# Kernel tuning notes

Hardware: AMD Instinct MI355X
Metric: run time of the kernel (lower is better)

Reference implementation:

```python
import jax, jax.numpy as jnp
import numpy as np

MD = 2        # max_displacement
STRIDE2 = 2   # displacement grid stride -> shifts in {-2, 0, 2}


def conv3x3_same(x, w):
    # x: [B,C,H,W], w: [O,I,3,3], stride 1, padding 1, no bias
    return jax.lax.conv_general_dilated(
        x, w, window_strides=(1, 1), padding=((1, 1), (1, 1)),
        dimension_numbers=("NCHW", "OIHW", "NCHW"))


def correlation(f1, f2):
    # FlowNet-style correlation, kernel_size=1: for each displacement (dy,dx)
    # in {-MD..MD step STRIDE2}^2, per-pixel channel dot product of f1 with
    # shifted f2, normalized by C (sumelems = kernel_size^2 * C).
    B, C, H, W = f1.shape
    f2p = jnp.pad(f2, ((0, 0), (0, 0), (MD, MD), (MD, MD)))
    outs = []
    for dy in range(-MD, MD + 1, STRIDE2):
        for dx in range(-MD, MD + 1, STRIDE2):
            f2s = f2p[:, :, MD + dy:MD + dy + H, MD + dx:MD + dx + W]
            outs.append(jnp.mean(f1 * f2s, axis=1))  # [B,H,W]
    return jnp.stack(outs, axis=1)  # [B, 9, H, W]


def setup_inputs() -> dict:
    key = jax.random.key(0)
    k1, k2, k3 = jax.random.split(key, 3)
    B, C, H, W = 16, 3, 512, 512
    x1 = jax.random.normal(k1, (B, C, H, W), dtype=jnp.float32)
    x2 = jax.random.normal(k2, (B, C, H, W), dtype=jnp.float32)
    # conv1: Conv2d(3, 3, kernel_size=3, bias=False); kaiming-ish scale
    fan_in = C * 3 * 3
    conv_w = jax.random.normal(k3, (3, C, 3, 3), dtype=jnp.float32) * np.float32(np.sqrt(2.0 / fan_in))
    return {"x1": x1, "x2": x2, "conv_w": conv_w}


def reference(x1, x2, conv_w):
    f1 = conv3x3_same(x1, conv_w)
    f2 = conv3x3_same(x2, conv_w)
    return correlation(f1, f2)  # [B, 9, H, W]
```

## Files before the change

kernel.cpp:

```cpp
#include <hip/hip_runtime.h>


#define HH 512
#define WW 512
#define TS 32
#define X2R 38
#define X2S 40
#define X1R 34
#define X1S 36
#define F2R 36
#define F2S 40
#define N2 (3*X2R*X2S)
#define N1 (3*X1R*X1S)
#define NC2 (3*X2R*(X2S/4))
#define NC1 (3*X1R*(X1S/4))

typedef const __attribute__((address_space(1))) void* gas_ptr;
typedef __attribute__((address_space(3))) void* las_ptr;
typedef float f32x4 __attribute__((ext_vector_type(4)));

__global__ __launch_bounds__(256)
void flownetc_fused_kernel(const float* __restrict__ x1,
                           const float* __restrict__ x2,
                           const float* __restrict__ cw,
                           float* __restrict__ out) {
  __shared__ __align__(16) float s_x2[N2];
  __shared__ __align__(16) float s_x1[N1];
  __shared__ __align__(16) float s_f2[3*F2R*F2S];

  const int tid = threadIdx.x;
  const int bid = blockIdx.x;
  const int f   = (bid & 7) * 512 + (bid >> 3);
  const int ox0 = (f & 15) * TS;
  const int oy0 = ((f >> 4) & 15) * TS;
  const int bi  = f >> 8;

  const float* x2b = x2 + (size_t)bi * 3 * HH * WW;
  const float* x1b = x1 + (size_t)bi * 3 * HH * WW;

  for (int q = tid; q < NC2; q += 256) {
    const int colq = q % (X2S / 4);
    const int rp   = q / (X2S / 4);
    const int r    = rp % X2R;
    const int c    = rp / X2R;
    const int gy   = oy0 - 3 + r;
    const int gx0  = ox0 - 3 + colq * 4;
    const float* src = x2b + (size_t)(c * HH + gy) * WW + gx0;
    if ((unsigned)gy < HH && (unsigned)gx0 <= (WW - 4)) {
      __builtin_amdgcn_global_load_lds((gas_ptr)src,
          (las_ptr)(s_x2 + ((q & ~63) << 2)), 16, 0, 0);
    } else {
      const bool rowok = (unsigned)gy < HH;
      float4 v;
      v.x = (rowok && (unsigned)(gx0 + 0) < WW) ? src[0] : 0.f;
      v.y = (rowok && (unsigned)(gx0 + 1) < WW) ? src[1] : 0.f;
      v.z = (rowok && (unsigned)(gx0 + 2) < WW) ? src[2] : 0.f;
      v.w = (rowok && (unsigned)(gx0 + 3) < WW) ? src[3] : 0.f;
      *reinterpret_cast<float4*>(&s_x2[q * 4]) = v;
    }
  }
  for (int q = tid; q < NC1; q += 256) {
    const int colq = q % (X1S / 4);
    const int rp   = q / (X1S / 4);
    const int r    = rp % X1R;
    const int c    = rp / X1R;
    const int gy   = oy0 - 1 + r;
    const int gx0  = ox0 - 1 + colq * 4;
    const float* src = x1b + (size_t)(c * HH + gy) * WW + gx0;
    if ((unsigned)gy < HH && (unsigned)gx0 <= (WW - 4)) {
      __builtin_amdgcn_global_load_lds((gas_ptr)src,
          (las_ptr)(s_x1 + ((q & ~63) << 2)), 16, 0, 0);
    } else {
      const bool rowok = (unsigned)gy < HH;
      float4 v;
      v.x = (rowok && (unsigned)(gx0 + 0) < WW) ? src[0] : 0.f;
      v.y = (rowok && (unsigned)(gx0 + 1) < WW) ? src[1] : 0.f;
      v.z = (rowok && (unsigned)(gx0 + 2) < WW) ? src[2] : 0.f;
      v.w = (rowok && (unsigned)(gx0 + 3) < WW) ? src[3] : 0.f;
      *reinterpret_cast<float4*>(&s_x1[q * 4]) = v;
    }
  }
  __syncthreads();

  for (int run = tid; run < 324; run += 256) {
    const int col0 = (run % 9) * 4;
    const int r    = run / 9;
    float acc[3][4] = {};
    #pragma unroll
    for (int ci = 0; ci < 3; ++ci) {
      float win[3][6];
      #pragma unroll
      for (int ky = 0; ky < 3; ++ky) {
        const float* base = &s_x2[(ci * X2R + r + ky) * X2S + col0];
        const float4 a  = *reinterpret_cast<const float4*>(base);
        const float2 b2 = *reinterpret_cast<const float2*>(base + 4);
        win[ky][0] = a.x; win[ky][1] = a.y; win[ky][2] = a.z; win[ky][3] = a.w;
        win[ky][4] = b2.x; win[ky][5] = b2.y;
      }
      #pragma unroll
      for (int co = 0; co < 3; ++co)
        #pragma unroll
        for (int ky = 0; ky < 3; ++ky)
          #pragma unroll
          for (int kx = 0; kx < 3; ++kx) {
            const float w = cw[((co * 3 + ci) * 3 + ky) * 3 + kx];
            #pragma unroll
            for (int j = 0; j < 4; ++j)
              acc[co][j] += w * win[ky][j + kx];
          }
    }
    const int gy = oy0 - 2 + r;
    #pragma unroll
    for (int j = 0; j < 4; ++j) {
      const int gx = ox0 - 2 + col0 + j;
      if (!((unsigned)gy < HH && (unsigned)gx < WW)) {
        acc[0][j] = 0.f; acc[1][j] = 0.f; acc[2][j] = 0.f;
      }
    }
    #pragma unroll
    for (int co = 0; co < 3; ++co)
      *reinterpret_cast<float4*>(&s_f2[(co * F2R + r) * F2S + col0]) =
          make_float4(acc[co][0], acc[co][1], acc[co][2], acc[co][3]);
  }

  const int py  = tid >> 3;
  const int px0 = (tid & 7) << 2;
  float f1r[3][4] = {};
  #pragma unroll
  for (int ci = 0; ci < 3; ++ci) {
    float win[3][6];
    #pragma unroll
    for (int ky = 0; ky < 3; ++ky) {
      const float* base = &s_x1[(ci * X1R + py + ky) * X1S + px0];
      const float4 a  = *reinterpret_cast<const float4*>(base);
      const float2 b2 = *reinterpret_cast<const float2*>(base + 4);
      win[ky][0] = a.x; win[ky][1] = a.y; win[ky][2] = a.z; win[ky][3] = a.w;
      win[ky][4] = b2.x; win[ky][5] = b2.y;
    }
    #pragma unroll
    for (int co = 0; co < 3; ++co)
      #pragma unroll
      for (int ky = 0; ky < 3; ++ky)
        #pragma unroll
        for (int kx = 0; kx < 3; ++kx) {
          const float w = cw[((co * 3 + ci) * 3 + ky) * 3 + kx];
          #pragma unroll
          for (int j = 0; j < 4; ++j)
            f1r[co][j] += w * win[ky][j + kx];
        }
  }
  __syncthreads();

  float* outp = out + ((size_t)bi * 9 * HH + (oy0 + py)) * WW + ox0 + px0;
  #pragma unroll
  for (int dyi = 0; dyi < 3; ++dyi) {
    float rv[3][8];
    #pragma unroll
    for (int c = 0; c < 3; ++c) {
      const float* base = &s_f2[(c * F2R + py + dyi * 2) * F2S + px0];
      const float4 a = *reinterpret_cast<const float4*>(base);
      const float4 b = *reinterpret_cast<const float4*>(base + 4);
      rv[c][0] = a.x; rv[c][1] = a.y; rv[c][2] = a.z; rv[c][3] = a.w;
      rv[c][4] = b.x; rv[c][5] = b.y; rv[c][6] = b.z; rv[c][7] = b.w;
    }
    #pragma unroll
    for (int dxi = 0; dxi < 3; ++dxi) {
      const int s = dxi * 2;
      f32x4 o;
      o.x = (f1r[0][0]*rv[0][s+0] + f1r[1][0]*rv[1][s+0] + f1r[2][0]*rv[2][s+0]) * (1.f/3.f);
      o.y = (f1r[0][1]*rv[0][s+1] + f1r[1][1]*rv[1][s+1] + f1r[2][1]*rv[2][s+1]) * (1.f/3.f);
      o.z = (f1r[0][2]*rv[0][s+2] + f1r[1][2]*rv[1][s+2] + f1r[2][2]*rv[2][s+2]) * (1.f/3.f);
      o.w = (f1r[0][3]*rv[0][s+3] + f1r[1][3]*rv[1][s+3] + f1r[2][3]*rv[2][s+3]) * (1.f/3.f);
      __builtin_nontemporal_store(o,
          reinterpret_cast<f32x4*>(outp + (size_t)(dyi * 3 + dxi) * HH * WW));
    }
  }
}

extern "C" void kernel_launch(void* const* d_in, const int* in_sizes, int n_in,
                              void* d_out, int out_size, void* d_ws, size_t ws_size,
                              hipStream_t stream) {
  const float* x1 = (const float*)d_in[0];
  const float* x2 = (const float*)d_in[1];
  const float* cw = (const float*)d_in[2];
  float* out = (float*)d_out;

  flownetc_fused_kernel<<<dim3(4096), 256, 0, stream>>>(x1, x2, cw, out);
}
```

Before: 62.03 us.

## Widen tiles to 64x32 with 512 threads and alias x1/f2 shared buffers

Doubles the tile width to 64 columns with 512-thread blocks, which cuts the relative halo overhead of loading x2/x1 and recomputing the f2 convolution on the border. The x1 staging buffer and the f2 result buffer now share one LDS array: f1 is computed first, then after a barrier f2 is written over it. This keeps LDS per block small despite the wider tile. It also folds the 1/3 mean scale into f1 once instead of applying it per output. The cost is an extra __syncthreads, more registers per thread under 512-thread launch bounds, and fewer blocks in the grid.

```diff
diff --git a/kernel.cpp b/kernel.cpp
--- a/kernel.cpp
+++ b/kernel.cpp
@@ -3,135 +3,101 @@
 
 #define HH 512
 #define WW 512
-#define TS 32
+#define TSX 64
+#define TSY 32
 #define X2R 38
-#define X2S 40
+#define X2S 72
 #define X1R 34
-#define X1S 36
+#define X1S 68
 #define F2R 36
-#define F2S 40
-#define N2 (3*X2R*X2S)
-#define N1 (3*X1R*X1S)
+#define F2S 68
 #define NC2 (3*X2R*(X2S/4))
 #define NC1 (3*X1R*(X1S/4))
+#define NFU (F2R*(F2S/4))
 
 typedef const __attribute__((address_space(1))) void* gas_ptr;
 typedef __attribute__((address_space(3))) void* las_ptr;
 typedef float f32x4 __attribute__((ext_vector_type(4)));
 
-__global__ __launch_bounds__(256)
+__global__ __launch_bounds__(512)
 void flownetc_fused_kernel(const float* __restrict__ x1,
                            const float* __restrict__ x2,
                            const float* __restrict__ cw,
                            float* __restrict__ out) {
-  __shared__ __align__(16) float s_x2[N2];
-  __shared__ __align__(16) float s_x1[N1];
-  __shared__ __align__(16) float s_f2[3*F2R*F2S];
+  __shared__ __align__(16) float s_x2[3*X2R*X2S];
+  __shared__ __align__(16) float s_ov[3*F2R*F2S];
 
   const int tid = threadIdx.x;
   const int bid = blockIdx.x;
-  const int f   = (bid & 7) * 512 + (bid >> 3);
-  const int ox0 = (f & 15) * TS;
-  const int oy0 = ((f >> 4) & 15) * TS;
-  const int bi  = f >> 8;
+  const int f   = (bid & 7) * 256 + (bid >> 3);
+  const int ox0 = (f & 7) * TSX;
+  const int oy0 = ((f >> 3) & 15) * TSY;
+  const int bi  = f >> 7;
 
   const float* x2b = x2 + (size_t)bi * 3 * HH * WW;
   const float* x1b = x1 + (size_t)bi * 3 * HH * WW;
 
-  for (int q = tid; q < NC2; q += 256) {
-    const int colq = q % (X2S / 4);
-    const int rp   = q / (X2S / 4);
-    const int r    = rp % X2R;
-    const int c    = rp / X2R;
-    const int gy   = oy0 - 3 + r;
-    const int gx0  = ox0 - 3 + colq * 4;
-    const float* src = x2b + (size_t)(c * HH + gy) * WW + gx0;
-    if ((unsigned)gy < HH && (unsigned)gx0 <= (WW - 4)) {
-      __builtin_amdgcn_global_load_lds((gas_ptr)src,
-          (las_ptr)(s_x2 + ((q & ~63) << 2)), 16, 0, 0);
-    } else {
-      const bool rowok = (unsigned)gy < HH;
-      float4 v;
-      v.x = (rowok && (unsigned)(gx0 + 0) < WW) ? src[0] : 0.f;
-      v.y = (rowok && (unsigned)(gx0 + 1) < WW) ? src[1] : 0.f;
-      v.z = (rowok && (unsigned)(gx0 + 2) < WW) ? src[2] : 0.f;
-      v.w = (rowok && (unsigned)(gx0 + 3) < WW) ? src[3] : 0.f;
-      *reinterpret_cast<float4*>(&s_x2[q * 4]) = v;
-    }
-  }
-  for (int q = tid; q < NC1; q += 256) {
-    const int colq = q % (X1S / 4);
-    const int rp   = q / (X1S / 4);
-    const int r    = rp % X1R;
-    const int c    = rp / X1R;
-    const int gy   = oy0 - 1 + r;
-    const int gx0  = ox0 - 1 + colq * 4;
-    const float* src = x1b + (size_t)(c * HH + gy) * WW + gx0;
-    if ((unsigned)gy < HH && (unsigned)gx0 <= (WW - 4)) {
-      __builtin_amdgcn_global_load_lds((gas_ptr)src,
-          (las_ptr)(s_x1 + ((q & ~63) << 2)), 16, 0, 0);
-    } else {
-      const bool rowok = (unsigned)gy < HH;
-      float4 v;
-      v.x = (rowok && (unsigned)(gx0 + 0) < WW) ? src[0] : 0.f;
-      v.y = (rowok && (unsigned)(gx0 + 1) < WW) ? src[1] : 0.f;
-      v.z = (rowok && (unsigned)(gx0 + 2) < WW) ? src[2] : 0.f;
-      v.w = (rowok && (unsigned)(gx0 + 3) < WW) ? src[3] : 0.f;
-      *reinterpret_cast<float4*>(&s_x1[q * 4]) = v;
+  #pragma unroll
+  for (int it = 0; it < 5; ++it) {
+    const int q = it * 512 + tid;
+    if (q < NC2) {
+      const int colq = q % (X2S / 4);
+      const int rp   = q / (X2S / 4);
+      const int r    = rp % X2R;
+      const int c    = rp / X2R;
+      const int gy   = oy0 - 3 + r;
+      const int gx0  = ox0 - 3 + colq * 4;
+      const float* src = x2b + (size_t)(c * HH + gy) * WW + gx0;
+      if ((unsigned)gy < HH && (unsigned)gx0 <= (WW - 4)) {
+        __builtin_amdgcn_global_load_lds((gas_ptr)src,
+            (las_ptr)(s_x2 + ((q & ~63) << 2)), 16, 0, 0);
+      } else {
+        const bool rowok = (unsigned)gy < HH;
+        float4 v;
+        v.x = (rowok && (unsigned)(gx0 + 0) < WW) ? src[0] : 0.f;
+        v.y = (rowok && (unsigned)(gx0 + 1) < WW) ? src[1] : 0.f;
+        v.z = (rowok && (unsigned)(gx0 + 2) < WW) ? src[2] : 0.f;
+        v.w = (rowok && (unsigned)(gx0 + 3) < WW) ? src[3] : 0.f;
+        *reinterpret_cast<float4*>(&s_x2[q * 4]) = v;
+      }
+    }
+  }
+  #pragma unroll
+  for (int it = 0; it < 4; ++it) {
+    const int q = it * 512 + tid;
+    if (q < NC1) {
+      const int colq = q % (X1S / 4);
+      const int rp   = q / (X1S / 4);
+      const int r    = rp % X1R;
+      const int c    = rp / X1R;
+      const int gy   = oy0 - 1 + r;
+      const int gx0  = ox0 - 1 + colq * 4;
+      const float* src = x1b + (size_t)(c * HH + gy) * WW + gx0;
+      if ((unsigned)gy < HH && (unsigned)gx0 <= (WW - 4)) {
+        __builtin_amdgcn_global_load_lds((gas_ptr)src,
+            (las_ptr)(s_ov + ((q & ~63) << 2)), 16, 0, 0);
+      } else {
+        const bool rowok = (unsigned)gy < HH;
+        float4 v;
+        v.x = (rowok && (unsigned)(gx0 + 0) < WW) ? src[0] : 0.f;
+        v.y = (rowok && (unsigned)(gx0 + 1) < WW) ? src[1] : 0.f;
+        v.z = (rowok && (unsigned)(gx0 + 2) < WW) ? src[2] : 0.f;
+        v.w = (rowok && (unsigned)(gx0 + 3) < WW) ? src[3] : 0.f;
+        *reinterpret_cast<float4*>(&s_ov[q * 4]) = v;
+      }
     }
   }
   __syncthreads();
 
-  for (int run = tid; run < 324; run += 256) {
-    const int col0 = (run % 9) * 4;
-    const int r    = run / 9;
-    float acc[3][4] = {};
-    #pragma unroll
-    for (int ci = 0; ci < 3; ++ci) {
-      float win[3][6];
-      #pragma unroll
-      for (int ky = 0; ky < 3; ++ky) {
-        const float* base = &s_x2[(ci * X2R + r + ky) * X2S + col0];
-        const float4 a  = *reinterpret_cast<const float4*>(base);
-        const float2 b2 = *reinterpret_cast<const float2*>(base + 4);
-        win[ky][0] = a.x; win[ky][1] = a.y; win[ky][2] = a.z; win[ky][3] = a.w;
-        win[ky][4] = b2.x; win[ky][5] = b2.y;
-      }
-      #pragma unroll
-      for (int co = 0; co < 3; ++co)
-        #pragma unroll
-        for (int ky = 0; ky < 3; ++ky)
-          #pragma unroll
-          for (int kx = 0; kx < 3; ++kx) {
-            const float w = cw[((co * 3 + ci) * 3 + ky) * 3 + kx];
-            #pragma unroll
-            for (int j = 0; j < 4; ++j)
-              acc[co][j] += w * win[ky][j + kx];
-          }
-    }
-    const int gy = oy0 - 2 + r;
-    #pragma unroll
-    for (int j = 0; j < 4; ++j) {
-      const int gx = ox0 - 2 + col0 + j;
-      if (!((unsigned)gy < HH && (unsigned)gx < WW)) {
-        acc[0][j] = 0.f; acc[1][j] = 0.f; acc[2][j] = 0.f;
-      }
-    }
-    #pragma unroll
-    for (int co = 0; co < 3; ++co)
-      *reinterpret_cast<float4*>(&s_f2[(co * F2R + r) * F2S + col0]) =
-          make_float4(acc[co][0], acc[co][1], acc[co][2], acc[co][3]);
-  }
-
-  const int py  = tid >> 3;
-  const int px0 = (tid & 7) << 2;
+  const int py  = tid >> 4;
+  const int px0 = (tid & 15) << 2;
   float f1r[3][4] = {};
   #pragma unroll
   for (int ci = 0; ci < 3; ++ci) {
     float win[3][6];
     #pragma unroll
     for (int ky = 0; ky < 3; ++ky) {
-      const float* base = &s_x1[(ci * X1R + py + ky) * X1S + px0];
+      const float* base = &s_ov[(ci * X1R + py + ky) * X1S + px0];
       const float4 a  = *reinterpret_cast<const float4*>(base);
       const float2 b2 = *reinterpret_cast<const float2*>(base + 4);
       win[ky][0] = a.x; win[ky][1] = a.y; win[ky][2] = a.z; win[ky][3] = a.w;
@@ -149,6 +115,57 @@
             f1r[co][j] += w * win[ky][j + kx];
         }
   }
+  #pragma unroll
+  for (int co = 0; co < 3; ++co)
+    #pragma unroll
+    for (int j = 0; j < 4; ++j)
+      f1r[co][j] *= (1.f / 3.f);
+  __syncthreads();
+
+  #pragma unroll
+  for (int half = 0; half < 2; ++half) {
+    const int u = half * 512 + tid;
+    if (u < NFU) {
+      const int col0 = (u % (F2S / 4)) * 4;
+      const int r    = u / (F2S / 4);
+      float acc[3][4] = {};
+      #pragma unroll
+      for (int ci = 0; ci < 3; ++ci) {
+        float win[3][6];
+        #pragma unroll
+        for (int ky = 0; ky < 3; ++ky) {
+          const float* base = &s_x2[(ci * X2R + r + ky) * X2S + col0];
+          const float4 a  = *reinterpret_cast<const float4*>(base);
+          const float2 b2 = *reinterpret_cast<const float2*>(base + 4);
+          win[ky][0] = a.x; win[ky][1] = a.y; win[ky][2] = a.z; win[ky][3] = a.w;
+          win[ky][4] = b2.x; win[ky][5] = b2.y;
+        }
+        #pragma unroll
+        for (int co = 0; co < 3; ++co)
+          #pragma unroll
+          for (int ky = 0; ky < 3; ++ky)
+            #pragma unroll
+            for (int kx = 0; kx < 3; ++kx) {
+              const float w = cw[((co * 3 + ci) * 3 + ky) * 3 + kx];
+              #pragma unroll
+              for (int j = 0; j < 4; ++j)
+                acc[co][j] += w * win[ky][j + kx];
+            }
+      }
+      const int gy = oy0 - 2 + r;
+      #pragma unroll
+      for (int j = 0; j < 4; ++j) {
+        const int gx = ox0 - 2 + col0 + j;
+        if (!((unsigned)gy < HH && (unsigned)gx < WW)) {
+          acc[0][j] = 0.f; acc[1][j] = 0.f; acc[2][j] = 0.f;
+        }
+      }
+      #pragma unroll
+      for (int co = 0; co < 3; ++co)
+        *reinterpret_cast<float4*>(&s_ov[(co * F2R + r) * F2S + col0]) =
+            make_float4(acc[co][0], acc[co][1], acc[co][2], acc[co][3]);
+    }
+  }
   __syncthreads();
 
   float* outp = out + ((size_t)bi * 9 * HH + (oy0 + py)) * WW + ox0 + px0;
@@ -157,7 +174,7 @@
     float rv[3][8];
     #pragma unroll
     for (int c = 0; c < 3; ++c) {
-      const float* base = &s_f2[(c * F2R + py + dyi * 2) * F2S + px0];
+      const float* base = &s_ov[(c * F2R + py + dyi * 2) * F2S + px0];
       const float4 a = *reinterpret_cast<const float4*>(base);
       const float4 b = *reinterpret_cast<const float4*>(base + 4);
       rv[c][0] = a.x; rv[c][1] = a.y; rv[c][2] = a.z; rv[c][3] = a.w;
@@ -167,10 +184,10 @@
     for (int dxi = 0; dxi < 3; ++dxi) {
       const int s = dxi * 2;
       f32x4 o;
-      o.x = (f1r[0][0]*rv[0][s+0] + f1r[1][0]*rv[1][s+0] + f1r[2][0]*rv[2][s+0]) * (1.f/3.f);
-      o.y = (f1r[0][1]*rv[0][s+1] + f1r[1][1]*rv[1][s+1] + f1r[2][1]*rv[2][s+1]) * (1.f/3.f);
-      o.z = (f1r[0][2]*rv[0][s+2] + f1r[1][2]*rv[1][s+2] + f1r[2][2]*rv[2][s+2]) * (1.f/3.f);
-      o.w = (f1r[0][3]*rv[0][s+3] + f1r[1][3]*rv[1][s+3] + f1r[2][3]*rv[2][s+3]) * (1.f/3.f);
+      o.x = f1r[0][0]*rv[0][s+0] + f1r[1][0]*rv[1][s+0] + f1r[2][0]*rv[2][s+0];
+      o.y = f1r[0][1]*rv[0][s+1] + f1r[1][1]*rv[1][s+1] + f1r[2][1]*rv[2][s+1];
+      o.z = f1r[0][2]*rv[0][s+2] + f1r[1][2]*rv[1][s+2] + f1r[2][2]*rv[2][s+2];
+      o.w = f1r[0][3]*rv[0][s+3] + f1r[1][3]*rv[1][s+3] + f1r[2][3]*rv[2][s+3];
       __builtin_nontemporal_store(o,
           reinterpret_cast<f32x4*>(outp + (size_t)(dyi * 3 + dxi) * HH * WW));
     }
@@ -185,5 +202,5 @@
   const float* cw = (const float*)d_in[2];
   float* out = (float*)d_out;
 
-  flownetc_fused_kernel<<<dim3(4096), 256, 0, stream>>>(x1, x2, cw, out);
+  flownetc_fused_kernel<<<dim3(2048), 512, 0, stream>>>(x1, x2, cw, out);
 }
```

After: 73.79 us. +19.0%, slower.

## Load x1 directly from global into registers and overlap f1 conv with x2 staging

Applied to the files above, without the earlier changes.

Removes the shared-memory staging of the x1 tile. Each thread now reads its x1 window straight from global memory using clamped indices and zero masks, and computes f1 before the first barrier so that work overlaps the asynchronous x2 LDS loads. The 1/3 normalization is folded into f1 once instead of being applied per output. The change reduces LDS usage, which may raise occupancy, at the cost of redundant, partially unaligned global loads for the x1 halo.

```diff
diff --git a/kernel.cpp b/kernel.cpp
--- a/kernel.cpp
+++ b/kernel.cpp
@@ -6,14 +6,10 @@
 #define TS 32
 #define X2R 38
 #define X2S 40
-#define X1R 34
-#define X1S 36
 #define F2R 36
 #define F2S 40
-#define N2 (3*X2R*X2S)
-#define N1 (3*X1R*X1S)
 #define NC2 (3*X2R*(X2S/4))
-#define NC1 (3*X1R*(X1S/4))
+#define NFU (F2R*9)
 
 typedef const __attribute__((address_space(1))) void* gas_ptr;
 typedef __attribute__((address_space(3))) void* las_ptr;
@@ -24,8 +20,7 @@
                            const float* __restrict__ x2,
                            const float* __restrict__ cw,
                            float* __restrict__ out) {
-  __shared__ __align__(16) float s_x2[N2];
-  __shared__ __align__(16) float s_x1[N1];
+  __shared__ __align__(16) float s_x2[3*X2R*X2S];
   __shared__ __align__(16) float s_f2[3*F2R*F2S];
 
   const int tid = threadIdx.x;
@@ -59,32 +54,56 @@
       *reinterpret_cast<float4*>(&s_x2[q * 4]) = v;
     }
   }
-  for (int q = tid; q < NC1; q += 256) {
-    const int colq = q % (X1S / 4);
-    const int rp   = q / (X1S / 4);
-    const int r    = rp % X1R;
-    const int c    = rp / X1R;
-    const int gy   = oy0 - 1 + r;
-    const int gx0  = ox0 - 1 + colq * 4;
-    const float* src = x1b + (size_t)(c * HH + gy) * WW + gx0;
-    if ((unsigned)gy < HH && (unsigned)gx0 <= (WW - 4)) {
-      __builtin_amdgcn_global_load_lds((gas_ptr)src,
-          (las_ptr)(s_x1 + ((q & ~63) << 2)), 16, 0, 0);
-    } else {
-      const bool rowok = (unsigned)gy < HH;
-      float4 v;
-      v.x = (rowok && (unsigned)(gx0 + 0) < WW) ? src[0] : 0.f;
-      v.y = (rowok && (unsigned)(gx0 + 1) < WW) ? src[1] : 0.f;
-      v.z = (rowok && (unsigned)(gx0 + 2) < WW) ? src[2] : 0.f;
-      v.w = (rowok && (unsigned)(gx0 + 3) < WW) ? src[3] : 0.f;
-      *reinterpret_cast<float4*>(&s_x1[q * 4]) = v;
+
+  const int py  = tid >> 3;
+  const int px0 = (tid & 7) << 2;
+  const int gx0 = ox0 + px0;
+  const int lidx = (gx0 == 0)       ? 0      : gx0 - 1;
+  const int ridx = (gx0 >= WW - 4)  ? WW - 1 : gx0 + 4;
+  const float mLc = (gx0 > 0)      ? 1.f : 0.f;
+  const float mRc = (gx0 < WW - 4) ? 1.f : 0.f;
+  float f1r[3][4] = {};
+  #pragma unroll
+  for (int ci = 0; ci < 3; ++ci) {
+    float win[3][6];
+    #pragma unroll
+    for (int ky = 0; ky < 3; ++ky) {
+      const int gy  = oy0 + py - 1 + ky;
+      const int gyc = gy < 0 ? 0 : (gy >= HH ? HH - 1 : gy);
+      const float mrow = ((unsigned)gy < HH) ? 1.f : 0.f;
+      const float* p = x1b + (size_t)(ci * HH + gyc) * WW;
+      const float4 A = *reinterpret_cast<const float4*>(p + gx0);
+      const float Lv = p[lidx];
+      const float Rv = p[ridx];
+      win[ky][0] = (mLc * mrow) * Lv;
+      win[ky][1] = mrow * A.x;
+      win[ky][2] = mrow * A.y;
+      win[ky][3] = mrow * A.z;
+      win[ky][4] = mrow * A.w;
+      win[ky][5] = (mRc * mrow) * Rv;
     }
+    #pragma unroll
+    for (int co = 0; co < 3; ++co)
+      #pragma unroll
+      for (int ky = 0; ky < 3; ++ky)
+        #pragma unroll
+        for (int kx = 0; kx < 3; ++kx) {
+          const float w = cw[((co * 3 + ci) * 3 + ky) * 3 + kx];
+          #pragma unroll
+          for (int j = 0; j < 4; ++j)
+            f1r[co][j] += w * win[ky][j + kx];
+        }
   }
+  #pragma unroll
+  for (int co = 0; co < 3; ++co)
+    #pragma unroll
+    for (int j = 0; j < 4; ++j)
+      f1r[co][j] *= (1.f / 3.f);
   __syncthreads();
 
-  for (int run = tid; run < 324; run += 256) {
-    const int col0 = (run % 9) * 4;
-    const int r    = run / 9;
+  for (int u = tid; u < NFU; u += 256) {
+    const int r    = u / 9;
+    const int col0 = (u - r * 9) * 4;
     float acc[3][4] = {};
     #pragma unroll
     for (int ci = 0; ci < 3; ++ci) {
@@ -122,36 +141,9 @@
       *reinterpret_cast<float4*>(&s_f2[(co * F2R + r) * F2S + col0]) =
           make_float4(acc[co][0], acc[co][1], acc[co][2], acc[co][3]);
   }
-
-  const int py  = tid >> 3;
-  const int px0 = (tid & 7) << 2;
-  float f1r[3][4] = {};
-  #pragma unroll
-  for (int ci = 0; ci < 3; ++ci) {
-    float win[3][6];
-    #pragma unroll
-    for (int ky = 0; ky < 3; ++ky) {
-      const float* base = &s_x1[(ci * X1R + py + ky) * X1S + px0];
-      const float4 a  = *reinterpret_cast<const float4*>(base);
-      const float2 b2 = *reinterpret_cast<const float2*>(base + 4);
-      win[ky][0] = a.x; win[ky][1] = a.y; win[ky][2] = a.z; win[ky][3] = a.w;
-      win[ky][4] = b2.x; win[ky][5] = b2.y;
-    }
-    #pragma unroll
-    for (int co = 0; co < 3; ++co)
-      #pragma unroll
-      for (int ky = 0; ky < 3; ++ky)
-        #pragma unroll
-        for (int kx = 0; kx < 3; ++kx) {
-          const float w = cw[((co * 3 + ci) * 3 + ky) * 3 + kx];
-          #pragma unroll
-          for (int j = 0; j < 4; ++j)
-            f1r[co][j] += w * win[ky][j + kx];
-        }
-  }
   __syncthreads();
 
-  float* outp = out + ((size_t)bi * 9 * HH + (oy0 + py)) * WW + ox0 + px0;
+  float* outp = out + ((size_t)bi * 9 * HH + (oy0 + py)) * WW + gx0;
   #pragma unroll
   for (int dyi = 0; dyi < 3; ++dyi) {
     float rv[3][8];
@@ -167,10 +159,10 @@
     for (int dxi = 0; dxi < 3; ++dxi) {
       const int s = dxi * 2;
       f32x4 o;
-      o.x = (f1r[0][0]*rv[0][s+0] + f1r[1][0]*rv[1][s+0] + f1r[2][0]*rv[2][s+0]) * (1.f/3.f);
-      o.y = (f1r[0][1]*rv[0][s+1] + f1r[1][1]*rv[1][s+1] + f1r[2][1]*rv[2][s+1]) * (1.f/3.f);
-      o.z = (f1r[0][2]*rv[0][s+2] + f1r[1][2]*rv[1][s+2] + f1r[2][2]*rv[2][s+2]) * (1.f/3.f);
-      o.w = (f1r[0][3]*rv[0][s+3] + f1r[1][3]*rv[1][s+3] + f1r[2][3]*rv[2][s+3]) * (1.f/3.f);
+      o.x = f1r[0][0]*rv[0][s+0] + f1r[1][0]*rv[1][s+0] + f1r[2][0]*rv[2][s+0];
+      o.y = f1r[0][1]*rv[0][s+1] + f1r[1][1]*rv[1][s+1] + f1r[2][1]*rv[2][s+1];
+      o.z = f1r[0][2]*rv[0][s+2] + f1r[1][2]*rv[1][s+2] + f1r[2][2]*rv[2][s+2];
+      o.w = f1r[0][3]*rv[0][s+3] + f1r[1][3]*rv[1][s+3] + f1r[2][3]*rv[2][s+3];
       __builtin_nontemporal_store(o,
           reinterpret_cast<f32x4*>(outp + (size_t)(dyi * 3 + dxi) * HH * WW));
     }
```

New measurement: 82.37 us. 32.8% more time.
